# Kernel tuning notes

Hardware: AMD Instinct MI355X
Metric: run time of the kernel (lower is better)

## Reference

```python
import jax, jax.numpy as jnp
import numpy as np

N = 100000   # nodes
E = 3200000  # directed edges
F = 32       # node features
H = 64       # hidden_channel


def _lin_params(k, fin, fout):
    k1, k2 = jax.random.split(k)
    s = 1.0 / np.sqrt(fin)
    W = jax.random.uniform(k1, (fin, fout), jnp.float32, -s, s)
    b = jax.random.uniform(k2, (fout,), jnp.float32, -s, s)
    return W, b


def setup_inputs() -> dict:
    key = jax.random.key(0)
    ks = jax.random.split(key, 8)
    x = jax.random.normal(ks[0], (N, F), jnp.float32)
    edges = jax.random.randint(ks[1], (E, 2), 0, N)  # [E,2] (src,dst) rows
    W1, b1 = _lin_params(ks[2], F, H)
    W2, b2 = _lin_params(ks[3], H + F, H)
    W3, b3 = _lin_params(ks[4], H + F, H)
    W4, b4 = _lin_params(ks[5], H + F, H)
    Wl1, bl1 = _lin_params(ks[6], H + F, H)
    Wl2, bl2 = _lin_params(ks[7], H + F, 1)  # num_classes==2 -> 1 sigmoid head
    return {"x": x, "edges": edges,
            "W1": W1, "b1": b1, "W2": W2, "b2": b2,
            "W3": W3, "b3": b3, "W4": W4, "b4": b4,
            "Wl1": Wl1, "bl1": bl1, "Wl2": Wl2, "bl2": bl2}


def reference(x, edges, W1, b1, W2, b2, W3, b3, W4, b4, Wl1, bl1, Wl2, bl2):
    n = x.shape[0]
    loop = jnp.arange(n)
    # GCN with self-loops; edge_index[0]=src, edge_index[1]=dst (PyG convention)
    src = jnp.concatenate([edges[:, 0], loop])
    dst = jnp.concatenate([edges[:, 1], loop])
    deg = jax.ops.segment_sum(jnp.ones(src.shape[0], x.dtype), dst, num_segments=n)
    dinv = jnp.where(deg > 0, jax.lax.rsqrt(jnp.maximum(deg, 1e-12)), 0.0)
    norm = dinv[src] * dinv[dst]  # [E+N]

    def gcn_conv(h, W, b):
        # transform first (small GEMM), then gather/scale/scatter-add
        msg = (h @ W)[src] * norm[:, None]           # [E+N, H]
        return jax.ops.segment_sum(msg, dst, num_segments=n) + b

    h = jax.nn.relu(gcn_conv(x, W1, b1))
    h = jax.nn.relu(gcn_conv(jnp.concatenate([x, h], -1), W2, b2))
    h = jax.nn.relu(gcn_conv(jnp.concatenate([x, h], -1), W3, b3))
    h = jax.nn.relu(gcn_conv(jnp.concatenate([x, h], -1), W4, b4))
    h = jax.nn.relu(jnp.concatenate([x, h], -1) @ Wl1 + bl1)
    out = jnp.concatenate([x, h], -1) @ Wl2 + bl2    # [N,1]
    return jax.nn.sigmoid(out).reshape(-1)           # flatten, num_classes==1
```

## Files before the change

### kernel.cpp

```cpp
#include <hip/hip_runtime.h>
#include <hip/hip_fp16.h>
#include <math.h>

#define TPB 256
#define BSHIFT 7
#define BNODES (1 << BSHIFT)
#define BMAX 1024
#define CH 4096
#define SPAN (4 * CH)
#define STAGE_CAP 6144

__global__ __launch_bounds__(256) void hist_kernel(const int2* __restrict__ edges,
                                                   int* __restrict__ bucket_cnt,
                                                   int e, int B) {
    __shared__ int h[BMAX];
    for (int i = threadIdx.x; i < B; i += 256) h[i] = 0;
    __syncthreads();
    for (int t = blockIdx.x * 256 + threadIdx.x; t < e; t += gridDim.x * 256)
        atomicAdd(&h[edges[t].y >> BSHIFT], 1);
    __syncthreads();
    for (int i = threadIdx.x; i < B; i += 256) {
        int c = h[i];
        if (c) atomicAdd(&bucket_cnt[i], c);
    }
}

__global__ __launch_bounds__(1024) void bscan_kernel(const int* __restrict__ bucket_cnt,
                                                     int* __restrict__ bucket_start,
                                                     int* __restrict__ bucket_cursor,
                                                     int* __restrict__ row_start,
                                                     int n, int e, int B) {
    __shared__ int s[BMAX];
    int t = threadIdx.x;
    s[t] = (t < B) ? bucket_cnt[t] : 0;
    __syncthreads();
    for (int off = 1; off < BMAX; off <<= 1) {
        int v = (t >= off) ? s[t - off] : 0;
        __syncthreads();
        s[t] += v;
        __syncthreads();
    }
    if (t < B) {
        int st = (t > 0) ? s[t - 1] : 0;
        bucket_start[t] = st;
        bucket_cursor[t] = st;
    }
    if (t == 0) { bucket_start[B] = e; row_start[n] = e; }
}

__global__ __launch_bounds__(256) void bin_kernel(const int2* __restrict__ edges,
                                                  int* __restrict__ bucket_cursor,
                                                  unsigned* __restrict__ ebuf,
                                                  int e, int B) {
    __shared__ int h[BMAX];
    long long start = (long long)blockIdx.x * SPAN;
    long long endS = start + SPAN < (long long)e ? start + SPAN : (long long)e;
    for (long long base = start; base < endS; base += CH) {
        int cnt = (int)((endS - base) < CH ? (endS - base) : CH);
        for (int i = threadIdx.x; i < B; i += 256) h[i] = 0;
        __syncthreads();
        for (int t = threadIdx.x; t < cnt; t += 256)
            atomicAdd(&h[edges[base + t].y >> BSHIFT], 1);
        __syncthreads();
        for (int i = threadIdx.x; i < B; i += 256) {
            int c = h[i];
            if (c) h[i] = atomicAdd(&bucket_cursor[i], c);
        }
        __syncthreads();
        for (int t = threadIdx.x; t < cnt; t += 256) {
            int2 sd = edges[base + t];
            int pos = atomicAdd(&h[sd.y >> BSHIFT], 1);
            ebuf[pos] = ((unsigned)(sd.y & (BNODES - 1)) << 17) | (unsigned)sd.x;
        }
        __syncthreads();
    }
}

__global__ __launch_bounds__(256) void finalize_kernel(const unsigned* __restrict__ ebuf,
                                                       const int* __restrict__ bucket_start,
                                                       int* __restrict__ row_start,
                                                       int* __restrict__ csr_src,
                                                       float* __restrict__ dinv, int n) {
    int b = blockIdx.x;
    int s0 = bucket_start[b], s1 = bucket_start[b + 1];
    int cnt = s1 - s0;
    int node0 = b << BSHIFT;
    int nn = min(BNODES, n - node0);
    __shared__ int ldeg[BNODES];
    __shared__ int lcur[BNODES];
    __shared__ int sc[BNODES];
    __shared__ unsigned stage[STAGE_CAP];
    int t = threadIdx.x;
    for (int i = t; i < BNODES; i += 256) ldeg[i] = 0;
    __syncthreads();
    bool uselds = (cnt <= STAGE_CAP);
    for (int tt = t; tt < cnt; tt += 256) {
        unsigned p = ebuf[s0 + tt];
        if (uselds) stage[tt] = p;
        atomicAdd(&ldeg[p >> 17], 1);
    }
    __syncthreads();
    if (t < BNODES) sc[t] = ldeg[t];
    __syncthreads();
    for (int off = 1; off < BNODES; off <<= 1) {
        int v = 0;
        if (t < BNODES && t >= off) v = sc[t - off];
        __syncthreads();
        if (t < BNODES) sc[t] += v;
        __syncthreads();
    }
    if (t < nn) {
        int excl = (t > 0) ? sc[t - 1] : 0;
        row_start[node0 + t] = s0 + excl;
        lcur[t] = s0 + excl;
        dinv[node0 + t] = rsqrtf((float)(ldeg[t] + 1));
    } else if (t < BNODES) {
        lcur[t] = 0;
    }
    __syncthreads();
    for (int tt = t; tt < cnt; tt += 256) {
        unsigned p = uselds ? stage[tt] : ebuf[s0 + tt];
        int pos = atomicAdd(&lcur[p >> 17], 1);
        csr_src[pos] = (int)(p & 0x1FFFFu);
    }
}

template <int FIN, int MODE>
__device__ __forceinline__ void accum4(const float4 v, const float* __restrict__ wk,
                                       float* __restrict__ res) {
#pragma unroll
    for (int cc = 0; cc < 16; cc++) res[cc] = fmaf(v.x, wk[cc], res[cc]);
#pragma unroll
    for (int cc = 0; cc < 16; cc++) res[cc] = fmaf(v.y, wk[64 + cc], res[cc]);
#pragma unroll
    for (int cc = 0; cc < 16; cc++) res[cc] = fmaf(v.z, wk[128 + cc], res[cc]);
#pragma unroll
    for (int cc = 0; cc < 16; cc++) res[cc] = fmaf(v.w, wk[192 + cc], res[cc]);
}

template <int FIN, int MODE>
__global__ __launch_bounds__(256) void gemm_node_k(
    const float* __restrict__ x, const float* __restrict__ h,
    const float* __restrict__ W, const float* __restrict__ bias,
    const float* __restrict__ dinv, void* __restrict__ out, int n) {
    int lane = threadIdx.x & 63;
    int wq = __builtin_amdgcn_readfirstlane(threadIdx.x >> 6);
    int node0 = blockIdx.x << 6;
    int i = node0 + lane;
    int ic = min(i, n - 1);
    float res[16];
#pragma unroll
    for (int cc = 0; cc < 16; cc++) res[cc] = 0.f;
    const float* Wq = W + wq * 16;
    const float4* xp = (const float4*)(x + (size_t)ic * 32);
#pragma unroll
    for (int q = 0; q < 8; q++)
        accum4<FIN, MODE>(xp[q], Wq + (size_t)(q * 4) * 64, res);
    if (FIN == 96) {
        const float4* hp = (const float4*)(h + (size_t)ic * 64);
#pragma unroll
        for (int q = 0; q < 16; q++)
            accum4<FIN, MODE>(hp[q], Wq + (size_t)(32 + q * 4) * 64, res);
    }
    if (MODE == 1) __syncthreads();
    if (i >= n) return;
    if (MODE == 0) {
        float scale = dinv[ic];
        union { unsigned short us[16]; uint4 v[2]; } u;
#pragma unroll
        for (int cc = 0; cc < 16; cc++)
            u.us[cc] = __half_as_ushort(__float2half(res[cc] * scale));
        uint4* dst = (uint4*)((unsigned short*)out + (size_t)i * 64 + wq * 16);
        dst[0] = u.v[0];
        dst[1] = u.v[1];
    } else {
        const float* bp = bias + wq * 16;
        float4* dst = (float4*)((float*)out + (size_t)i * 64 + wq * 16);
#pragma unroll
        for (int t4 = 0; t4 < 4; t4++) {
            float4 o;
            o.x = fmaxf(res[t4 * 4 + 0] + bp[t4 * 4 + 0], 0.f);
            o.y = fmaxf(res[t4 * 4 + 1] + bp[t4 * 4 + 1], 0.f);
            o.z = fmaxf(res[t4 * 4 + 2] + bp[t4 * 4 + 2], 0.f);
            o.w = fmaxf(res[t4 * 4 + 3] + bp[t4 * 4 + 3], 0.f);
            dst[t4] = o;
        }
    }
}

__device__ __forceinline__ void acc8(const uint4 v, float* a) {
    float2 f;
    f = __half22float2(*(const __half2*)&v.x); a[0] += f.x; a[1] += f.y;
    f = __half22float2(*(const __half2*)&v.y); a[2] += f.x; a[3] += f.y;
    f = __half22float2(*(const __half2*)&v.z); a[4] += f.x; a[5] += f.y;
    f = __half22float2(*(const __half2*)&v.w); a[6] += f.x; a[7] += f.y;
}

__global__ __launch_bounds__(256) void aggregate_h(
    const uint4* __restrict__ Tsh4, const int* __restrict__ row_start,
    const int* __restrict__ csr_src, const float* __restrict__ dinv,
    const float* __restrict__ bias, float* __restrict__ hout, int n) {
    int i = blockIdx.x * 32 + (threadIdx.x >> 3);
    if (i >= n) return;
    int q = threadIdx.x & 7;
    float accA[8], accB[8], accC[8], accD[8];
#pragma unroll
    for (int k = 0; k < 8; k++) { accB[k] = 0.f; accC[k] = 0.f; accD[k] = 0.f; }
    {
        uint4 sv = Tsh4[(size_t)i * 8 + q];
        float2 f;
        f = __half22float2(*(const __half2*)&sv.x); accA[0] = f.x; accA[1] = f.y;
        f = __half22float2(*(const __half2*)&sv.y); accA[2] = f.x; accA[3] = f.y;
        f = __half22float2(*(const __half2*)&sv.z); accA[4] = f.x; accA[5] = f.y;
        f = __half22float2(*(const __half2*)&sv.w); accA[6] = f.x; accA[7] = f.y;
    }
    int s0 = row_start[i], s1 = row_start[i + 1];
    int j = s0;
    for (; j + 4 <= s1; j += 4) {
        int sa = csr_src[j], sb = csr_src[j + 1];
        int sc_ = csr_src[j + 2], sd = csr_src[j + 3];
        uint4 va = Tsh4[(size_t)sa * 8 + q];
        uint4 vb = Tsh4[(size_t)sb * 8 + q];
        uint4 vc = Tsh4[(size_t)sc_ * 8 + q];
        uint4 vd = Tsh4[(size_t)sd * 8 + q];
        acc8(va, accA);
        acc8(vb, accB);
        acc8(vc, accC);
        acc8(vd, accD);
    }
    for (; j < s1; j++) {
        int sa = csr_src[j];
        acc8(Tsh4[(size_t)sa * 8 + q], accA);
    }
    float di = dinv[i];
    const float4* bp = (const float4*)(bias + q * 8);
    float4 b0 = bp[0], b1 = bp[1];
    float4 o0, o1;
    o0.x = fmaxf((accA[0] + accB[0] + accC[0] + accD[0]) * di + b0.x, 0.f);
    o0.y = fmaxf((accA[1] + accB[1] + accC[1] + accD[1]) * di + b0.y, 0.f);
    o0.z = fmaxf((accA[2] + accB[2] + accC[2] + accD[2]) * di + b0.z, 0.f);
    o0.w = fmaxf((accA[3] + accB[3] + accC[3] + accD[3]) * di + b0.w, 0.f);
    o1.x = fmaxf((accA[4] + accB[4] + accC[4] + accD[4]) * di + b1.x, 0.f);
    o1.y = fmaxf((accA[5] + accB[5] + accC[5] + accD[5]) * di + b1.y, 0.f);
    o1.z = fmaxf((accA[6] + accB[6] + accC[6] + accD[6]) * di + b1.z, 0.f);
    o1.w = fmaxf((accA[7] + accB[7] + accC[7] + accD[7]) * di + b1.w, 0.f);
    float4* op = (float4*)(hout + (size_t)i * 64 + q * 8);
    op[0] = o0;
    op[1] = o1;
}

__global__ __launch_bounds__(256) void final_kernel(
    const float* __restrict__ x, const float* __restrict__ h5,
    const float* __restrict__ Wl2, const float* __restrict__ bl2,
    float* __restrict__ out, int n) {
    int i = blockIdx.x * TPB + threadIdx.x;
    if (i >= n) return;
    float acc = bl2[0];
#pragma unroll
    for (int k = 0; k < 32; k++) acc = fmaf(x[(size_t)i * 32 + k], Wl2[k], acc);
#pragma unroll
    for (int k = 0; k < 64; k++) acc = fmaf(h5[(size_t)i * 64 + k], Wl2[32 + k], acc);
    out[i] = 1.f / (1.f + expf(-acc));
}

extern "C" void kernel_launch(void* const* d_in, const int* in_sizes, int n_in,
                              void* d_out, int out_size, void* d_ws, size_t ws_size,
                              hipStream_t stream) {
    const float* x   = (const float*)d_in[0];
    const int*   edg = (const int*)d_in[1];
    const float* W1  = (const float*)d_in[2];
    const float* b1  = (const float*)d_in[3];
    const float* W2  = (const float*)d_in[4];
    const float* b2  = (const float*)d_in[5];
    const float* W3  = (const float*)d_in[6];
    const float* b3  = (const float*)d_in[7];
    const float* W4  = (const float*)d_in[8];
    const float* b4  = (const float*)d_in[9];
    const float* Wl1 = (const float*)d_in[10];
    const float* bl1 = (const float*)d_in[11];
    const float* Wl2 = (const float*)d_in[12];
    const float* bl2 = (const float*)d_in[13];
    int n = in_sizes[0] / 32;
    int e = in_sizes[1] / 2;
    int B = (n + BNODES - 1) >> BSHIFT;

    char* ws = (char*)d_ws;
    size_t off = 0;
    auto take = [&](size_t bytes) {
        char* p = ws + off;
        off = (off + bytes + 255) & ~(size_t)255;
        return p;
    };
    int*   bucket_cnt    = (int*)take((size_t)B * 4);
    int*   bucket_start  = (int*)take((size_t)(B + 1) * 4);
    int*   bucket_cursor = (int*)take((size_t)B * 4);
    int*   row_start     = (int*)take((size_t)(n + 1) * 4);
    int*   csr_src       = (int*)take((size_t)e * 4);
    float* dinv          = (float*)take((size_t)n * 4);
    unsigned* Tsh        = (unsigned*)take((size_t)n * 64 * 2);
    float* hbuf          = (float*)take((size_t)n * 64 * 4);
    unsigned* ebuf = (unsigned*)Tsh;

    hipMemsetAsync(bucket_cnt, 0, (size_t)B * 4, stream);

    int nb = (n + TPB - 1) / TPB;
    int nspans = (e + SPAN - 1) / SPAN;
    hist_kernel<<<512, 256, 0, stream>>>((const int2*)edg, bucket_cnt, e, B);
    bscan_kernel<<<1, 1024, 0, stream>>>(bucket_cnt, bucket_start, bucket_cursor,
                                         row_start, n, e, B);
    bin_kernel<<<nspans, 256, 0, stream>>>((const int2*)edg, bucket_cursor, ebuf, e, B);
    finalize_kernel<<<B, 256, 0, stream>>>(ebuf, bucket_start, row_start, csr_src, dinv, n);

    int gb = (n + 63) / 64;
    int ab = (n + 31) / 32;

    gemm_node_k<32, 0><<<gb, TPB, 0, stream>>>(x, nullptr, W1, nullptr, dinv, Tsh, n);
    aggregate_h<<<ab, TPB, 0, stream>>>((const uint4*)Tsh, row_start, csr_src, dinv, b1, hbuf, n);
    gemm_node_k<96, 0><<<gb, TPB, 0, stream>>>(x, hbuf, W2, nullptr, dinv, Tsh, n);
    aggregate_h<<<ab, TPB, 0, stream>>>((const uint4*)Tsh, row_start, csr_src, dinv, b2, hbuf, n);
    gemm_node_k<96, 0><<<gb, TPB, 0, stream>>>(x, hbuf, W3, nullptr, dinv, Tsh, n);
    aggregate_h<<<ab, TPB, 0, stream>>>((const uint4*)Tsh, row_start, csr_src, dinv, b3, hbuf, n);
    gemm_node_k<96, 0><<<gb, TPB, 0, stream>>>(x, hbuf, W4, nullptr, dinv, Tsh, n);
    aggregate_h<<<ab, TPB, 0, stream>>>((const uint4*)Tsh, row_start, csr_src, dinv, b4, hbuf, n);
    gemm_node_k<96, 1><<<gb, TPB, 0, stream>>>(x, hbuf, Wl1, bl1, dinv, hbuf, n);
    final_kernel<<<nb, TPB, 0, stream>>>(x, hbuf, Wl2, bl2, (float*)d_out, n);
}
```

Baseline: 558.3 us.

## Split node features into 16-channel planes and aggregate one plane per thread

Feature buffers are reorganized into four planar 16-channel slices, and the aggregation kernel assigns one thread per node per plane, with blocks interleaved across planes. This aims to shrink the per-pass gather working set for better cache hit rates and to avoid intra-row lane splitting. In exchange, CSR indices are reread four times and each thread serially walks its full neighbor list with less unrolling, which may expose more latency and load imbalance.

Result: slower. 1.010 ms (+80.8%).

```diff
diff --git a/kernel.cpp b/kernel.cpp
--- a/kernel.cpp
+++ b/kernel.cpp
@@ -152,15 +152,34 @@
 #pragma unroll
     for (int cc = 0; cc < 16; cc++) res[cc] = 0.f;
     const float* Wq = W + wq * 16;
+    float xr[FIN];
     const float4* xp = (const float4*)(x + (size_t)ic * 32);
 #pragma unroll
+    for (int q = 0; q < 8; q++) {
+        float4 v = xp[q];
+        xr[q * 4] = v.x; xr[q * 4 + 1] = v.y; xr[q * 4 + 2] = v.z; xr[q * 4 + 3] = v.w;
+    }
+    if (FIN == 96) {
+#pragma unroll
+        for (int pp = 0; pp < 4; pp++) {
+            const float4* hp = (const float4*)(h + ((size_t)pp * n + ic) * 16);
+#pragma unroll
+            for (int q = 0; q < 4; q++) {
+                float4 v = hp[q];
+                xr[32 + pp * 16 + q * 4] = v.x; xr[32 + pp * 16 + q * 4 + 1] = v.y;
+                xr[32 + pp * 16 + q * 4 + 2] = v.z; xr[32 + pp * 16 + q * 4 + 3] = v.w;
+            }
+        }
+    }
+#pragma unroll
     for (int q = 0; q < 8; q++)
-        accum4<FIN, MODE>(xp[q], Wq + (size_t)(q * 4) * 64, res);
+        accum4<FIN, MODE>(make_float4(xr[q*4], xr[q*4+1], xr[q*4+2], xr[q*4+3]),
+                          Wq + (size_t)(q * 4) * 64, res);
     if (FIN == 96) {
-        const float4* hp = (const float4*)(h + (size_t)ic * 64);
-#pragma unroll
-        for (int q = 0; q < 16; q++)
-            accum4<FIN, MODE>(hp[q], Wq + (size_t)(32 + q * 4) * 64, res);
+#pragma unroll
+        for (int q = 8; q < 24; q++)
+            accum4<FIN, MODE>(make_float4(xr[q*4], xr[q*4+1], xr[q*4+2], xr[q*4+3]),
+                              Wq + (size_t)(q * 4) * 64, res);
     }
     if (MODE == 1) __syncthreads();
     if (i >= n) return;
@@ -170,12 +189,12 @@
 #pragma unroll
         for (int cc = 0; cc < 16; cc++)
             u.us[cc] = __half_as_ushort(__float2half(res[cc] * scale));
-        uint4* dst = (uint4*)((unsigned short*)out + (size_t)i * 64 + wq * 16);
+        uint4* dst = (uint4*)out + ((size_t)wq * n + i) * 2;
         dst[0] = u.v[0];
         dst[1] = u.v[1];
     } else {
         const float* bp = bias + wq * 16;
-        float4* dst = (float4*)((float*)out + (size_t)i * 64 + wq * 16);
+        float4* dst = (float4*)((float*)out + ((size_t)wq * n + i) * 16);
 #pragma unroll
         for (int t4 = 0; t4 < 4; t4++) {
             float4 o;
@@ -196,61 +215,62 @@
     f = __half22float2(*(const __half2*)&v.w); a[6] += f.x; a[7] += f.y;
 }
 
-__global__ __launch_bounds__(256) void aggregate_h(
-    const uint4* __restrict__ Tsh4, const int* __restrict__ row_start,
+__global__ __launch_bounds__(256) void aggregate_p(
+    const uint4* __restrict__ Tp, const int* __restrict__ row_start,
     const int* __restrict__ csr_src, const float* __restrict__ dinv,
-    const float* __restrict__ bias, float* __restrict__ hout, int n) {
-    int i = blockIdx.x * 32 + (threadIdx.x >> 3);
+    const float* __restrict__ bias, float* __restrict__ houtp, int n) {
+    int p = blockIdx.x & 3;
+    int i = (blockIdx.x >> 2) * 256 + threadIdx.x;
     if (i >= n) return;
-    int q = threadIdx.x & 7;
-    float accA[8], accB[8], accC[8], accD[8];
-#pragma unroll
-    for (int k = 0; k < 8; k++) { accB[k] = 0.f; accC[k] = 0.f; accD[k] = 0.f; }
+    size_t pbase = (size_t)p * n;
+    float accA[16], accB[16];
+#pragma unroll
+    for (int k = 0; k < 16; k++) accB[k] = 0.f;
     {
-        uint4 sv = Tsh4[(size_t)i * 8 + q];
+        uint4 s0v = Tp[(pbase + i) * 2];
+        uint4 s1v = Tp[(pbase + i) * 2 + 1];
         float2 f;
-        f = __half22float2(*(const __half2*)&sv.x); accA[0] = f.x; accA[1] = f.y;
-        f = __half22float2(*(const __half2*)&sv.y); accA[2] = f.x; accA[3] = f.y;
-        f = __half22float2(*(const __half2*)&sv.z); accA[4] = f.x; accA[5] = f.y;
-        f = __half22float2(*(const __half2*)&sv.w); accA[6] = f.x; accA[7] = f.y;
+        f = __half22float2(*(const __half2*)&s0v.x); accA[0] = f.x; accA[1] = f.y;
+        f = __half22float2(*(const __half2*)&s0v.y); accA[2] = f.x; accA[3] = f.y;
+        f = __half22float2(*(const __half2*)&s0v.z); accA[4] = f.x; accA[5] = f.y;
+        f = __half22float2(*(const __half2*)&s0v.w); accA[6] = f.x; accA[7] = f.y;
+        f = __half22float2(*(const __half2*)&s1v.x); accA[8] = f.x; accA[9] = f.y;
+        f = __half22float2(*(const __half2*)&s1v.y); accA[10] = f.x; accA[11] = f.y;
+        f = __half22float2(*(const __half2*)&s1v.z); accA[12] = f.x; accA[13] = f.y;
+        f = __half22float2(*(const __half2*)&s1v.w); accA[14] = f.x; accA[15] = f.y;
     }
     int s0 = row_start[i], s1 = row_start[i + 1];
     int j = s0;
-    for (; j + 4 <= s1; j += 4) {
+    for (; j + 2 <= s1; j += 2) {
         int sa = csr_src[j], sb = csr_src[j + 1];
-        int sc_ = csr_src[j + 2], sd = csr_src[j + 3];
-        uint4 va = Tsh4[(size_t)sa * 8 + q];
-        uint4 vb = Tsh4[(size_t)sb * 8 + q];
-        uint4 vc = Tsh4[(size_t)sc_ * 8 + q];
-        uint4 vd = Tsh4[(size_t)sd * 8 + q];
-        acc8(va, accA);
-        acc8(vb, accB);
-        acc8(vc, accC);
-        acc8(vd, accD);
-    }
-    for (; j < s1; j++) {
+        uint4 va0 = Tp[(pbase + sa) * 2];
+        uint4 va1 = Tp[(pbase + sa) * 2 + 1];
+        uint4 vb0 = Tp[(pbase + sb) * 2];
+        uint4 vb1 = Tp[(pbase + sb) * 2 + 1];
+        acc8(va0, accA); acc8(va1, accA + 8);
+        acc8(vb0, accB); acc8(vb1, accB + 8);
+    }
+    if (j < s1) {
         int sa = csr_src[j];
-        acc8(Tsh4[(size_t)sa * 8 + q], accA);
+        acc8(Tp[(pbase + sa) * 2], accA);
+        acc8(Tp[(pbase + sa) * 2 + 1], accA + 8);
     }
     float di = dinv[i];
-    const float4* bp = (const float4*)(bias + q * 8);
-    float4 b0 = bp[0], b1 = bp[1];
-    float4 o0, o1;
-    o0.x = fmaxf((accA[0] + accB[0] + accC[0] + accD[0]) * di + b0.x, 0.f);
-    o0.y = fmaxf((accA[1] + accB[1] + accC[1] + accD[1]) * di + b0.y, 0.f);
-    o0.z = fmaxf((accA[2] + accB[2] + accC[2] + accD[2]) * di + b0.z, 0.f);
-    o0.w = fmaxf((accA[3] + accB[3] + accC[3] + accD[3]) * di + b0.w, 0.f);
-    o1.x = fmaxf((accA[4] + accB[4] + accC[4] + accD[4]) * di + b1.x, 0.f);
-    o1.y = fmaxf((accA[5] + accB[5] + accC[5] + accD[5]) * di + b1.y, 0.f);
-    o1.z = fmaxf((accA[6] + accB[6] + accC[6] + accD[6]) * di + b1.z, 0.f);
-    o1.w = fmaxf((accA[7] + accB[7] + accC[7] + accD[7]) * di + b1.w, 0.f);
-    float4* op = (float4*)(hout + (size_t)i * 64 + q * 8);
-    op[0] = o0;
-    op[1] = o1;
+    const float* bp = bias + p * 16;
+    float4* op = (float4*)(houtp + (pbase + i) * 16);
+#pragma unroll
+    for (int t4 = 0; t4 < 4; t4++) {
+        float4 o;
+        o.x = fmaxf((accA[t4 * 4 + 0] + accB[t4 * 4 + 0]) * di + bp[t4 * 4 + 0], 0.f);
+        o.y = fmaxf((accA[t4 * 4 + 1] + accB[t4 * 4 + 1]) * di + bp[t4 * 4 + 1], 0.f);
+        o.z = fmaxf((accA[t4 * 4 + 2] + accB[t4 * 4 + 2]) * di + bp[t4 * 4 + 2], 0.f);
+        o.w = fmaxf((accA[t4 * 4 + 3] + accB[t4 * 4 + 3]) * di + bp[t4 * 4 + 3], 0.f);
+        op[t4] = o;
+    }
 }
 
 __global__ __launch_bounds__(256) void final_kernel(
-    const float* __restrict__ x, const float* __restrict__ h5,
+    const float* __restrict__ x, const float* __restrict__ h5p,
     const float* __restrict__ Wl2, const float* __restrict__ bl2,
     float* __restrict__ out, int n) {
     int i = blockIdx.x * TPB + threadIdx.x;
@@ -259,7 +279,12 @@
 #pragma unroll
     for (int k = 0; k < 32; k++) acc = fmaf(x[(size_t)i * 32 + k], Wl2[k], acc);
 #pragma unroll
-    for (int k = 0; k < 64; k++) acc = fmaf(h5[(size_t)i * 64 + k], Wl2[32 + k], acc);
+    for (int p = 0; p < 4; p++) {
+        const float* hp = h5p + ((size_t)p * n + i) * 16;
+#pragma unroll
+        for (int k = 0; k < 16; k++)
+            acc = fmaf(hp[k], Wl2[32 + p * 16 + k], acc);
+    }
     out[i] = 1.f / (1.f + expf(-acc));
 }
 
@@ -297,9 +322,9 @@
     int*   row_start     = (int*)take((size_t)(n + 1) * 4);
     int*   csr_src       = (int*)take((size_t)e * 4);
     float* dinv          = (float*)take((size_t)n * 4);
-    unsigned* Tsh        = (unsigned*)take((size_t)n * 64 * 2);
-    float* hbuf          = (float*)take((size_t)n * 64 * 4);
-    unsigned* ebuf = (unsigned*)Tsh;
+    unsigned* Tshp       = (unsigned*)take((size_t)n * 64 * 2);
+    float* hbufp         = (float*)take((size_t)n * 64 * 4);
+    unsigned* ebuf = (unsigned*)Tshp;
 
     hipMemsetAsync(bucket_cnt, 0, (size_t)B * 4, stream);
 
@@ -312,16 +337,16 @@
     finalize_kernel<<<B, 256, 0, stream>>>(ebuf, bucket_start, row_start, csr_src, dinv, n);
 
     int gb = (n + 63) / 64;
-    int ab = (n + 31) / 32;
-
-    gemm_node_k<32, 0><<<gb, TPB, 0, stream>>>(x, nullptr, W1, nullptr, dinv, Tsh, n);
-    aggregate_h<<<ab, TPB, 0, stream>>>((const uint4*)Tsh, row_start, csr_src, dinv, b1, hbuf, n);
-    gemm_node_k<96, 0><<<gb, TPB, 0, stream>>>(x, hbuf, W2, nullptr, dinv, Tsh, n);
-    aggregate_h<<<ab, TPB, 0, stream>>>((const uint4*)Tsh, row_start, csr_src, dinv, b2, hbuf, n);
-    gemm_node_k<96, 0><<<gb, TPB, 0, stream>>>(x, hbuf, W3, nullptr, dinv, Tsh, n);
-    aggregate_h<<<ab, TPB, 0, stream>>>((const uint4*)Tsh, row_start, csr_src, dinv, b3, hbuf, n);
-    gemm_node_k<96, 0><<<gb, TPB, 0, stream>>>(x, hbuf, W4, nullptr, dinv, Tsh, n);
-    aggregate_h<<<ab, TPB, 0, stream>>>((const uint4*)Tsh, row_start, csr_src, dinv, b4, hbuf, n);
-    gemm_node_k<96, 1><<<gb, TPB, 0, stream>>>(x, hbuf, Wl1, bl1, dinv, hbuf, n);
-    final_kernel<<<nb, TPB, 0, stream>>>(x, hbuf, Wl2, bl2, (float*)d_out, n);
-}
+    int ab = 4 * ((n + 255) / 256);
+
+    gemm_node_k<32, 0><<<gb, TPB, 0, stream>>>(x, nullptr, W1, nullptr, dinv, Tshp, n);
+    aggregate_p<<<ab, TPB, 0, stream>>>((const uint4*)Tshp, row_start, csr_src, dinv, b1, hbufp, n);
+    gemm_node_k<96, 0><<<gb, TPB, 0, stream>>>(x, hbufp, W2, nullptr, dinv, Tshp, n);
+    aggregate_p<<<ab, TPB, 0, stream>>>((const uint4*)Tshp, row_start, csr_src, dinv, b2, hbufp, n);
+    gemm_node_k<96, 0><<<gb, TPB, 0, stream>>>(x, hbufp, W3, nullptr, dinv, Tshp, n);
+    aggregate_p<<<ab, TPB, 0, stream>>>((const uint4*)Tshp, row_start, csr_src, dinv, b3, hbufp, n);
+    gemm_node_k<96, 0><<<gb, TPB, 0, stream>>>(x, hbufp, W4, nullptr, dinv, Tshp, n);
+    aggregate_p<<<ab, TPB, 0, stream>>>((const uint4*)Tshp, row_start, csr_src, dinv, b4, hbufp, n);
+    gemm_node_k<96, 1><<<gb, TPB, 0, stream>>>(x, hbufp, Wl1, bl1, dinv, hbufp, n);
+    final_kernel<<<nb, TPB, 0, stream>>>(x, hbufp, Wl2, bl2, (float*)d_out, n);
+}
```
